# Kernel tuning notes

Hardware: AMD Instinct MI355X
Metric: run time of the kernel (lower is better)

Reference implementation:

```python
import jax, jax.numpy as jnp
import numpy as np

D = 256; NH = 8; NL = 4; NP = 4; DH = D // NH; DFFN = 1024; NQ = 900; BS = 4
SPATIAL = ((92, 92), (46, 46), (23, 23), (12, 12))  # (H, W) per level
LEVEL_START = (0, 8464, 10580, 11109)
S = sum(h * w for h, w in SPATIAL)  # 11253


def _ln(x, g, b):
    m = jnp.mean(x, -1, keepdims=True)
    v = jnp.var(x, -1, keepdims=True)
    return (x - m) / jnp.sqrt(v + 1e-5) * g + b


def setup_inputs() -> dict:
    key = jax.random.key(0)
    ks = jax.random.split(key, 24)
    p = lambda k, s: 0.02 * jax.random.normal(k, s, jnp.float32)
    return {
        "tgt": jax.random.normal(ks[0], (NQ, BS, D), jnp.float32),
        "tgt_query_pos": jax.random.normal(ks[1], (NQ, BS, D), jnp.float32),
        "tgt_reference_points": jax.random.uniform(ks[2], (NQ, BS, NL, 2), jnp.float32),
        "memory": jax.random.normal(ks[3], (S, BS, D), jnp.float32),
        "memory_spatial_shapes": jnp.array(SPATIAL, jnp.int32),
        "memory_level_start_index": jnp.array(LEVEL_START, jnp.int32),
        "in_proj_w": p(ks[4], (3 * D, D)), "in_proj_b": p(ks[5], (3 * D,)),
        "out_proj_w": p(ks[6], (D, D)), "out_proj_b": p(ks[7], (D,)),
        "off_w": p(ks[8], (NH * NL * NP * 2, D)), "off_b": p(ks[9], (NH * NL * NP * 2,)),
        "aw_w": p(ks[10], (NH * NL * NP, D)), "aw_b": p(ks[11], (NH * NL * NP,)),
        "vproj_w": p(ks[12], (D, D)), "vproj_b": p(ks[13], (D,)),
        "oproj_w": p(ks[14], (D, D)), "oproj_b": p(ks[15], (D,)),
        "ln1_g": jnp.ones((D,), jnp.float32), "ln1_b": jnp.zeros((D,), jnp.float32),
        "ln2_g": jnp.ones((D,), jnp.float32), "ln2_b": jnp.zeros((D,), jnp.float32),
        "ln3_g": jnp.ones((D,), jnp.float32), "ln3_b": jnp.zeros((D,), jnp.float32),
        "lin1_w": p(ks[16], (DFFN, D)), "lin1_b": p(ks[17], (DFFN,)),
        "lin2_w": p(ks[18], (D, DFFN)), "lin2_b": p(ks[19], (D,)),
    }


def _self_attn(q, k, v, in_w, in_b, out_w, out_b):
    # q, k, v: (nq, bs, d) -- torch nn.MultiheadAttention, eval mode
    wq, wk, wv = jnp.split(in_w, 3, axis=0)
    bq, bk, bv = jnp.split(in_b, 3)
    qp = (q @ wq.T + bq).reshape(NQ, BS, NH, DH)
    kp = (k @ wk.T + bk).reshape(NQ, BS, NH, DH)
    vp = (v @ wv.T + bv).reshape(NQ, BS, NH, DH)
    s = jnp.einsum("qbhd,kbhd->bhqk", qp, kp) / jnp.sqrt(jnp.float32(DH))
    a = jax.nn.softmax(s, axis=-1)
    o = jnp.einsum("bhqk,kbhd->qbhd", a, vp).reshape(NQ, BS, D)
    return o @ out_w.T + out_b


def _msdeform(x, ref, mem, off_w, off_b, aw_w, aw_b, vproj_w, vproj_b, oproj_w, oproj_b):
    # x: (bs, nq, d); ref: (bs, nq, nl, 2) in [0,1]; mem: (bs, S, d)
    value = (mem @ vproj_w.T + vproj_b).reshape(BS, S, NH, DH)
    off = (x @ off_w.T + off_b).reshape(BS, NQ, NH, NL, NP, 2)
    aw = jax.nn.softmax((x @ aw_w.T + aw_b).reshape(BS, NQ, NH, NL * NP), axis=-1)
    aw = aw.reshape(BS, NQ, NH, NL, NP)
    # offset normalizer = (W, H) per level
    norm = jnp.array([[w, h] for (h, w) in SPATIAL], jnp.float32)
    loc = ref[:, :, None, :, None, :] + off / norm[None, None, None, :, None, :]
    out = jnp.zeros((BS, NH, NQ, DH), x.dtype)
    for l, (H, W) in enumerate(SPATIAL):
        s0 = LEVEL_START[l]
        v = value[:, s0:s0 + H * W].transpose(0, 2, 1, 3)  # (bs, nh, H*W, dh)
        g = loc[:, :, :, l].transpose(0, 2, 1, 3, 4)       # (bs, nh, nq, np, 2)
        # grid_sample align_corners=False, padding_mode='zeros'
        px = g[..., 0] * W - 0.5
        py = g[..., 1] * H - 0.5
        x0 = jnp.floor(px).astype(jnp.int32)
        y0 = jnp.floor(py).astype(jnp.int32)
        wx = px - x0
        wy = py - y0
        samp = jnp.zeros((BS, NH, NQ, NP, DH), x.dtype)
        for dx, dy, w in ((0, 0, (1 - wx) * (1 - wy)), (1, 0, wx * (1 - wy)),
                          (0, 1, (1 - wx) * wy), (1, 1, wx * wy)):
            xi = x0 + dx
            yi = y0 + dy
            valid = ((xi >= 0) & (xi < W) & (yi >= 0) & (yi < H)).astype(x.dtype)
            idx = (jnp.clip(yi, 0, H - 1) * W + jnp.clip(xi, 0, W - 1)).reshape(BS, NH, NQ * NP)
            gat = jnp.take_along_axis(v, idx[..., None], axis=2).reshape(BS, NH, NQ, NP, DH)
            samp = samp + (w * valid)[..., None] * gat
        a = aw[:, :, :, l].transpose(0, 2, 1, 3)  # (bs, nh, nq, np)
        out = out + (samp * a[..., None]).sum(axis=3)
    out = out.transpose(0, 2, 1, 3).reshape(BS, NQ, D)
    return out @ oproj_w.T + oproj_b


def reference(tgt, tgt_query_pos, tgt_reference_points, memory,
              memory_spatial_shapes, memory_level_start_index,
              in_proj_w, in_proj_b, out_proj_w, out_proj_b,
              off_w, off_b, aw_w, aw_b, vproj_w, vproj_b, oproj_w, oproj_b,
              ln1_g, ln1_b, ln2_g, ln2_b, ln3_g, ln3_b,
              lin1_w, lin1_b, lin2_w, lin2_b):
    # module_seq = ['sa', 'ca', 'ffn']; dropout inactive (eval)
    q = tgt + tgt_query_pos
    tgt2 = _self_attn(q, q, tgt, in_proj_w, in_proj_b, out_proj_w, out_proj_b)
    tgt = _ln(tgt + tgt2, ln2_g, ln2_b)
    x = (tgt + tgt_query_pos).transpose(1, 0, 2)
    ref = tgt_reference_points.transpose(1, 0, 2, 3)
    mem = memory.transpose(1, 0, 2)
    tgt2 = _msdeform(x, ref, mem, off_w, off_b, aw_w, aw_b,
                     vproj_w, vproj_b, oproj_w, oproj_b).transpose(1, 0, 2)
    tgt = _ln(tgt + tgt2, ln1_g, ln1_b)
    ff = jax.nn.relu(tgt @ lin1_w.T + lin1_b) @ lin2_w.T + lin2_b
    return _ln(tgt + ff, ln3_g, ln3_b)
```

## Files before the change

kernel.cpp:

```cpp
#include <hip/hip_runtime.h>
#include <math.h>

#define D_MODEL 256
#define NHEAD   8
#define NLVL    4
#define NPTS    4
#define DHEAD   32
#define DFFN    1024
#define NQ      900
#define BSZ     4
#define NROW    (NQ * BSZ)
#define S_TOT   11253
#define VROWS   (S_TOT * BSZ)
#define SASCALE 0.17677669529663687f

typedef __attribute__((ext_vector_type(8))) short short8;
typedef __attribute__((ext_vector_type(4))) float f32x4;
typedef unsigned short ushort_t;

static __device__ __forceinline__ unsigned f2bf1(float f) {
    unsigned u = __float_as_uint(f);
    return (u + 0x7FFFu + ((u >> 16) & 1u)) >> 16;
}
static __device__ __forceinline__ unsigned pack2bf(float x, float y) {
    return f2bf1(x) | (f2bf1(y) << 16);
}
static __device__ __forceinline__ float bf2f(ushort_t u) {
    return __uint_as_float(((unsigned)u) << 16);
}

#define GPAD 72

__global__ __launch_bounds__(256) void qkv_fused(
    const float* __restrict__ tgt, const float* __restrict__ qpos,
    const float* __restrict__ W, const float* __restrict__ bias,
    ushort_t* __restrict__ C)
{
    __shared__ ushort_t As[64 * GPAD];
    __shared__ ushort_t Ws[64 * GPAD];

    const int t  = threadIdx.x;
    const int m0 = blockIdx.x * 64;
    const int n0 = blockIdx.y * 64;
    const bool addpos = (n0 < 512);
    const float oscale = (n0 < 256) ? SASCALE : 1.f;

    const int trow = t >> 2;
    const int tk   = (t & 3) << 4;
    const int wv   = t >> 6;
    const int ln   = t & 63;
    const int L    = ln & 15;
    const int quad = ln >> 4;

    f32x4 acc[4] = {{0.f,0.f,0.f,0.f},{0.f,0.f,0.f,0.f},
                    {0.f,0.f,0.f,0.f},{0.f,0.f,0.f,0.f}};

    for (int k0 = 0; k0 < 256; k0 += 64) {
        {
            int m = m0 + trow;
            float4 a0, a1, a2, a3;
            if (m < NROW) {
                const float* ap = tgt + (size_t)m * 256 + k0 + tk;
                a0 = *(const float4*)(ap + 0);
                a1 = *(const float4*)(ap + 4);
                a2 = *(const float4*)(ap + 8);
                a3 = *(const float4*)(ap + 12);
                if (addpos) {
                    const float* pp = qpos + (size_t)m * 256 + k0 + tk;
                    float4 p0 = *(const float4*)(pp + 0);
                    float4 p1 = *(const float4*)(pp + 4);
                    float4 p2 = *(const float4*)(pp + 8);
                    float4 p3 = *(const float4*)(pp + 12);
                    a0.x += p0.x; a0.y += p0.y; a0.z += p0.z; a0.w += p0.w;
                    a1.x += p1.x; a1.y += p1.y; a1.z += p1.z; a1.w += p1.w;
                    a2.x += p2.x; a2.y += p2.y; a2.z += p2.z; a2.w += p2.w;
                    a3.x += p3.x; a3.y += p3.y; a3.z += p3.z; a3.w += p3.w;
                }
            } else {
                a0 = a1 = a2 = a3 = make_float4(0.f, 0.f, 0.f, 0.f);
            }
            uint4 u0, u1;
            u0.x = pack2bf(a0.x, a0.y); u0.y = pack2bf(a0.z, a0.w);
            u0.z = pack2bf(a1.x, a1.y); u0.w = pack2bf(a1.z, a1.w);
            u1.x = pack2bf(a2.x, a2.y); u1.y = pack2bf(a2.z, a2.w);
            u1.z = pack2bf(a3.x, a3.y); u1.w = pack2bf(a3.z, a3.w);
            *(uint4*)&As[trow * GPAD + tk + 0] = u0;
            *(uint4*)&As[trow * GPAD + tk + 8] = u1;
        }
        {
            int n = n0 + trow;
            const float* wp = W + (size_t)n * 256 + k0 + tk;
            float4 a0 = *(const float4*)(wp + 0);
            float4 a1 = *(const float4*)(wp + 4);
            float4 a2 = *(const float4*)(wp + 8);
            float4 a3 = *(const float4*)(wp + 12);
            uint4 u0, u1;
            u0.x = pack2bf(a0.x, a0.y); u0.y = pack2bf(a0.z, a0.w);
            u0.z = pack2bf(a1.x, a1.y); u0.w = pack2bf(a1.z, a1.w);
            u1.x = pack2bf(a2.x, a2.y); u1.y = pack2bf(a2.z, a2.w);
            u1.z = pack2bf(a3.x, a3.y); u1.w = pack2bf(a3.z, a3.w);
            *(uint4*)&Ws[trow * GPAD + tk + 0] = u0;
            *(uint4*)&Ws[trow * GPAD + tk + 8] = u1;
        }
        __syncthreads();
#pragma unroll
        for (int kh = 0; kh < 2; ++kh) {
            short8 af = *(const short8*)&As[(wv * 16 + L) * GPAD + kh * 32 + quad * 8];
#pragma unroll
            for (int cb = 0; cb < 4; ++cb) {
                short8 bf = *(const short8*)&Ws[(cb * 16 + L) * GPAD + kh * 32 + quad * 8];
                acc[cb] = __builtin_amdgcn_mfma_f32_16x16x32_bf16(af, bf, acc[cb], 0, 0, 0);
            }
        }
        __syncthreads();
    }
#pragma unroll
    for (int cb = 0; cb < 4; ++cb) {
        int col = n0 + cb * 16 + L;
        float bv = bias[col];
#pragma unroll
        for (int i = 0; i < 4; ++i) {
            int m = m0 + wv * 16 + quad * 4 + i;
            if (m < NROW)
                C[(size_t)m * 768 + col] = (ushort_t)f2bf1((acc[cb][i] + bv) * oscale);
        }
    }
}

__global__ __launch_bounds__(256) void sa_flash16(
    const ushort_t* __restrict__ qkv, ushort_t* __restrict__ attn_out)
{
    __shared__ ushort_t Ks[2 * 2080];
    __shared__ ushort_t Vt[2 * 2304];
    __shared__ ushort_t Ps[4 * 1152];

    const int t    = threadIdx.x;
    const int q0   = blockIdx.x * 64;
    const int b    = blockIdx.y & 3;
    const int h    = blockIdx.y >> 2;
    const int wv   = t >> 6;
    const int ln   = t & 63;
    const int L    = ln & 15;
    const int quad = ln >> 4;

    union { uint4 u; short8 s; } qu;
    qu.u = make_uint4(0u, 0u, 0u, 0u);
    {
        int q = q0 + wv * 16 + L;
        if (q < NQ)
            qu.u = *(const uint4*)(qkv + ((size_t)q * 4 + b) * 768 + h * 32 + quad * 8);
    }
    const short8 qf = qu.s;

    float mrun = -1e30f, lrun = 0.f;
    f32x4 oacc[2] = {{0.f,0.f,0.f,0.f},{0.f,0.f,0.f,0.f}};

    const int skey = t >> 2;
    const int sdg  = t & 3;

    int it = 0;
    for (int k0 = 0; k0 < NQ; k0 += 64, it ^= 1) {
        {
            int kg = k0 + skey;
            uint4 ku = make_uint4(0u,0u,0u,0u), vu = make_uint4(0u,0u,0u,0u);
            if (kg < NQ) {
                const ushort_t* base = qkv + ((size_t)kg * 4 + b) * 768 + 256 + h * 32 + sdg * 8;
                ku = *(const uint4*)base;
                vu = *(const uint4*)(base + 256);
            }
            *(uint4*)&Ks[it * 2080 + sdg * 520 + skey * 8] = ku;
            ushort_t* vp = &Vt[it * 2304 + sdg * 8 * 72 + skey];
            vp[0 * 72] = (ushort_t)(vu.x & 0xffffu);
            vp[1 * 72] = (ushort_t)(vu.x >> 16);
            vp[2 * 72] = (ushort_t)(vu.y & 0xffffu);
            vp[3 * 72] = (ushort_t)(vu.y >> 16);
            vp[4 * 72] = (ushort_t)(vu.z & 0xffffu);
            vp[5 * 72] = (ushort_t)(vu.z >> 16);
            vp[6 * 72] = (ushort_t)(vu.w & 0xffffu);
            vp[7 * 72] = (ushort_t)(vu.w >> 16);
        }
        __syncthreads();

        f32x4 sacc[4] = {{0.f,0.f,0.f,0.f},{0.f,0.f,0.f,0.f},
                         {0.f,0.f,0.f,0.f},{0.f,0.f,0.f,0.f}};
#pragma unroll
        for (int cb = 0; cb < 4; ++cb) {
            short8 kf = *(const short8*)&Ks[it * 2080 + quad * 520 + (cb * 16 + L) * 8];
            sacc[cb] = __builtin_amdgcn_mfma_f32_16x16x32_bf16(kf, qf, sacc[cb], 0, 0, 0);
        }
        if (k0 + 64 > NQ) {
#pragma unroll
            for (int cb = 0; cb < 4; ++cb)
#pragma unroll
                for (int i = 0; i < 4; ++i)
                    if (k0 + cb * 16 + quad * 4 + i >= NQ) sacc[cb][i] = -1e30f;
        }

        float ml = -1e30f;
#pragma unroll
        for (int cb = 0; cb < 4; ++cb)
#pragma unroll
            for (int i = 0; i < 4; ++i) ml = fmaxf(ml, sacc[cb][i]);
        ml = fmaxf(ml, __shfl_xor(ml, 16, 64));
        ml = fmaxf(ml, __shfl_xor(ml, 32, 64));
        float mnew  = fmaxf(mrun, ml);
        float alpha = __expf(mrun - mnew);
        float p[16];
        float rs = 0.f;
#pragma unroll
        for (int cb = 0; cb < 4; ++cb)
#pragma unroll
            for (int i = 0; i < 4; ++i) {
                float e = __expf(sacc[cb][i] - mnew);
                p[cb * 4 + i] = e;
                rs += e;
            }
        rs += __shfl_xor(rs, 16, 64);
        rs += __shfl_xor(rs, 32, 64);
        lrun = lrun * alpha + rs;
        mrun = mnew;

        {
            ushort_t* pw = &Ps[wv * 1152 + L * 72];
#pragma unroll
            for (int cb = 0; cb < 4; ++cb) {
                uint2 u;
                u.x = pack2bf(p[cb * 4 + 0], p[cb * 4 + 1]);
                u.y = pack2bf(p[cb * 4 + 2], p[cb * 4 + 3]);
                *(uint2*)&pw[cb * 16 + quad * 4] = u;
            }
        }
#pragma unroll
        for (int i = 0; i < 4; ++i) {
            float ai = __shfl(alpha, quad * 4 + i, 64);
            oacc[0][i] *= ai;
            oacc[1][i] *= ai;
        }
        __syncthreads();

#pragma unroll
        for (int ks = 0; ks < 2; ++ks) {
            short8 pf = *(const short8*)&Ps[wv * 1152 + L * 72 + ks * 32 + quad * 8];
#pragma unroll
            for (int db = 0; db < 2; ++db) {
                short8 vf = *(const short8*)&Vt[it * 2304 + (db * 16 + L) * 72 + ks * 32 + quad * 8];
                oacc[db] = __builtin_amdgcn_mfma_f32_16x16x32_bf16(pf, vf, oacc[db], 0, 0, 0);
            }
        }
    }

#pragma unroll
    for (int i = 0; i < 4; ++i) {
        float lq = __shfl(lrun, quad * 4 + i, 64);
        float li = 1.f / lq;
        int q = q0 + wv * 16 + quad * 4 + i;
        if (q < NQ) {
            ushort_t* op = attn_out + ((size_t)q * 4 + b) * 256 + h * 32 + L;
            op[0]  = (ushort_t)f2bf1(oacc[0][i] * li);
            op[16] = (ushort_t)f2bf1(oacc[1][i] * li);
        }
    }
}

__global__ __launch_bounds__(256) void gemm16_f32(
    const ushort_t* __restrict__ A, const float* __restrict__ W,
    const float* __restrict__ bias, float* __restrict__ C,
    int M, int N, int K, int ldc)
{
    __shared__ ushort_t As[64 * GPAD];
    __shared__ ushort_t Ws[64 * GPAD];

    const int t  = threadIdx.x;
    const int m0 = blockIdx.x * 64;
    const int n0 = blockIdx.y * 64;
    const int trow = t >> 2;
    const int tk   = (t & 3) << 4;
    const int wv   = t >> 6;
    const int ln   = t & 63;
    const int L    = ln & 15;
    const int quad = ln >> 4;

    f32x4 acc[4] = {{0.f,0.f,0.f,0.f},{0.f,0.f,0.f,0.f},
                    {0.f,0.f,0.f,0.f},{0.f,0.f,0.f,0.f}};

    for (int k0 = 0; k0 < K; k0 += 64) {
        {
            int m = m0 + trow;
            uint4 a0 = make_uint4(0u,0u,0u,0u), a1 = make_uint4(0u,0u,0u,0u);
            if (m < M) {
                const ushort_t* ap = A + (size_t)m * K + k0 + tk;
                a0 = *(const uint4*)ap;
                a1 = *(const uint4*)(ap + 8);
            }
            *(uint4*)&As[trow * GPAD + tk + 0] = a0;
            *(uint4*)&As[trow * GPAD + tk + 8] = a1;
        }
        {
            int n = n0 + trow;
            const float* wp = W + (size_t)n * K + k0 + tk;
            float4 a0 = *(const float4*)(wp + 0);
            float4 a1 = *(const float4*)(wp + 4);
            float4 a2 = *(const float4*)(wp + 8);
            float4 a3 = *(const float4*)(wp + 12);
            uint4 u0, u1;
            u0.x = pack2bf(a0.x, a0.y); u0.y = pack2bf(a0.z, a0.w);
            u0.z = pack2bf(a1.x, a1.y); u0.w = pack2bf(a1.z, a1.w);
            u1.x = pack2bf(a2.x, a2.y); u1.y = pack2bf(a2.z, a2.w);
            u1.z = pack2bf(a3.x, a3.y); u1.w = pack2bf(a3.z, a3.w);
            *(uint4*)&Ws[trow * GPAD + tk + 0] = u0;
            *(uint4*)&Ws[trow * GPAD + tk + 8] = u1;
        }
        __syncthreads();
#pragma unroll
        for (int kh = 0; kh < 2; ++kh) {
            short8 af = *(const short8*)&As[(wv * 16 + L) * GPAD + kh * 32 + quad * 8];
#pragma unroll
            for (int cb = 0; cb < 4; ++cb) {
                short8 bf = *(const short8*)&Ws[(cb * 16 + L) * GPAD + kh * 32 + quad * 8];
                acc[cb] = __builtin_amdgcn_mfma_f32_16x16x32_bf16(af, bf, acc[cb], 0, 0, 0);
            }
        }
        __syncthreads();
    }
#pragma unroll
    for (int cb = 0; cb < 4; ++cb) {
        int col = n0 + cb * 16 + L;
        float bv = bias[col];
#pragma unroll
        for (int i = 0; i < 4; ++i) {
            int m = m0 + wv * 16 + quad * 4 + i;
            if (m < M)
                C[(size_t)m * ldc + col] = acc[cb][i] + bv;
        }
    }
}

__global__ __launch_bounds__(256) void ln_resid16(
    const float* __restrict__ xa, const float* __restrict__ xb,
    const float* __restrict__ gam, const float* __restrict__ bet,
    float* __restrict__ out, const float* __restrict__ pos,
    ushort_t* __restrict__ out2)
{
    const int row = blockIdx.x;
    const int t = threadIdx.x;
    float x = xa[(size_t)row * D_MODEL + t] + xb[(size_t)row * D_MODEL + t];
    float s = x, s2 = x * x;
#pragma unroll
    for (int off = 32; off > 0; off >>= 1) {
        s  += __shfl_down(s, off, 64);
        s2 += __shfl_down(s2, off, 64);
    }
    __shared__ float rs[4], rs2[4];
    __shared__ float mean_s, rstd_s;
    int wid = t >> 6, lane = t & 63;
    if (lane == 0) { rs[wid] = s; rs2[wid] = s2; }
    __syncthreads();
    if (t == 0) {
        float S = rs[0] + rs[1] + rs[2] + rs[3];
        float S2 = rs2[0] + rs2[1] + rs2[2] + rs2[3];
        float mean = S * (1.f / 256.f);
        float var = S2 * (1.f / 256.f) - mean * mean;
        mean_s = mean;
        rstd_s = rsqrtf(var + 1e-5f);
    }
    __syncthreads();
    float y = (x - mean_s) * rstd_s * gam[t] + bet[t];
    out[(size_t)row * D_MODEL + t] = y;
    if (out2) {
        float o2 = y + (pos ? pos[(size_t)row * D_MODEL + t] : 0.f);
        out2[(size_t)row * D_MODEL + t] = (ushort_t)f2bf1(o2);
    }
}

__global__ __launch_bounds__(256) void vproj_bf16(
    const float* __restrict__ A, const float* __restrict__ W,
    const float* __restrict__ bias, ushort_t* __restrict__ C, int M)
{
    __shared__ ushort_t As[64 * GPAD];
    __shared__ ushort_t Ws[256 * GPAD];

    const int t  = threadIdx.x;
    const int m0 = blockIdx.x * 64;
    const int trow = t >> 2;
    const int tk   = (t & 3) << 4;
    const int wv   = t >> 6;
    const int ln   = t & 63;
    const int L    = ln & 15;
    const int quad = ln >> 4;

    f32x4 acc[16];
#pragma unroll
    for (int i = 0; i < 16; ++i) acc[i] = (f32x4){0.f, 0.f, 0.f, 0.f};

    for (int k0 = 0; k0 < 256; k0 += 64) {
        {
            int m = m0 + trow;
            float4 a0, a1, a2, a3;
            if (m < M) {
                const float* ap = A + (size_t)m * 256 + k0 + tk;
                a0 = *(const float4*)(ap + 0);
                a1 = *(const float4*)(ap + 4);
                a2 = *(const float4*)(ap + 8);
                a3 = *(const float4*)(ap + 12);
            } else {
                a0 = a1 = a2 = a3 = make_float4(0.f, 0.f, 0.f, 0.f);
            }
            uint4 u0, u1;
            u0.x = pack2bf(a0.x, a0.y); u0.y = pack2bf(a0.z, a0.w);
            u0.z = pack2bf(a1.x, a1.y); u0.w = pack2bf(a1.z, a1.w);
            u1.x = pack2bf(a2.x, a2.y); u1.y = pack2bf(a2.z, a2.w);
            u1.z = pack2bf(a3.x, a3.y); u1.w = pack2bf(a3.z, a3.w);
            *(uint4*)&As[trow * GPAD + tk + 0] = u0;
            *(uint4*)&As[trow * GPAD + tk + 8] = u1;
        }
#pragma unroll
        for (int wb = 0; wb < 4; ++wb) {
            int n = wb * 64 + trow;
            const float* wp = W + (size_t)n * 256 + k0 + tk;
            float4 a0 = *(const float4*)(wp + 0);
            float4 a1 = *(const float4*)(wp + 4);
            float4 a2 = *(const float4*)(wp + 8);
            float4 a3 = *(const float4*)(wp + 12);
            uint4 u0, u1;
            u0.x = pack2bf(a0.x, a0.y); u0.y = pack2bf(a0.z, a0.w);
            u0.z = pack2bf(a1.x, a1.y); u0.w = pack2bf(a1.z, a1.w);
            u1.x = pack2bf(a2.x, a2.y); u1.y = pack2bf(a2.z, a2.w);
            u1.z = pack2bf(a3.x, a3.y); u1.w = pack2bf(a3.z, a3.w);
            *(uint4*)&Ws[n * GPAD + tk + 0] = u0;
            *(uint4*)&Ws[n * GPAD + tk + 8] = u1;
        }
        __syncthreads();
#pragma unroll
        for (int kh = 0; kh < 2; ++kh) {
            short8 af = *(const short8*)&As[(wv * 16 + L) * GPAD + kh * 32 + quad * 8];
#pragma unroll
            for (int cb = 0; cb < 16; ++cb) {
                short8 bf = *(const short8*)&Ws[(cb * 16 + L) * GPAD + kh * 32 + quad * 8];
                acc[cb] = __builtin_amdgcn_mfma_f32_16x16x32_bf16(af, bf, acc[cb], 0, 0, 0);
            }
        }
        __syncthreads();
    }

    ushort_t* Cs = Ws;
#pragma unroll
    for (int cb = 0; cb < 16; ++cb) {
        int col = cb * 16 + L;
        float bv = bias[col];
#pragma unroll
        for (int i = 0; i < 4; ++i) {
            int r = wv * 16 + quad * 4 + i;
            Cs[r * 264 + col] = (ushort_t)f2bf1(acc[cb][i] + bv);
        }
    }
    __syncthreads();
    {
        int r  = t >> 2;
        int ch = (t & 3) * 64;
        int m  = m0 + r;
        if (m < M) {
            const ushort_t* src = &Cs[r * 264 + ch];
            uint4* dst = (uint4*)(C + (size_t)m * 256 + ch);
#pragma unroll
            for (int j = 0; j < 8; ++j)
                dst[j] = *(const uint4*)(src + j * 8);
        }
    }
}

__global__ __launch_bounds__(256) void offaw16(
    const ushort_t* __restrict__ A,
    const float* __restrict__ off_w, const float* __restrict__ off_b,
    const float* __restrict__ aw_w, const float* __restrict__ aw_b,
    float* __restrict__ off_raw, float* __restrict__ aw_raw)
{
    __shared__ ushort_t As[64 * GPAD];
    __shared__ ushort_t Ws[64 * GPAD];

    const int t  = threadIdx.x;
    const int m0 = blockIdx.x * 64;
    const int by = blockIdx.y;
    const bool isaw = (by >= 4);
    const int n0 = isaw ? (by - 4) * 64 : by * 64;
    const float* W  = isaw ? aw_w : off_w;
    const float* bs = isaw ? aw_b : off_b;
    float* C = isaw ? aw_raw : off_raw;
    const int ldc = isaw ? 128 : 256;

    const int trow = t >> 2;
    const int tk   = (t & 3) << 4;
    const int wv   = t >> 6;
    const int ln   = t & 63;
    const int L    = ln & 15;
    const int quad = ln >> 4;

    f32x4 acc[4] = {{0.f,0.f,0.f,0.f},{0.f,0.f,0.f,0.f},
                    {0.f,0.f,0.f,0.f},{0.f,0.f,0.f,0.f}};

    for (int k0 = 0; k0 < 256; k0 += 64) {
        {
            int m = m0 + trow;
            uint4 a0 = make_uint4(0u,0u,0u,0u), a1 = make_uint4(0u,0u,0u,0u);
            if (m < NROW) {
                const ushort_t* ap = A + (size_t)m * 256 + k0 + tk;
                a0 = *(const uint4*)ap;
                a1 = *(const uint4*)(ap + 8);
            }
            *(uint4*)&As[trow * GPAD + tk + 0] = a0;
            *(uint4*)&As[trow * GPAD + tk + 8] = a1;
        }
        {
            int n = n0 + trow;
            const float* wp = W + (size_t)n * 256 + k0 + tk;
            float4 a0 = *(const float4*)(wp + 0);
            float4 a1 = *(const float4*)(wp + 4);
            float4 a2 = *(const float4*)(wp + 8);
            float4 a3 = *(const float4*)(wp + 12);
            uint4 u0, u1;
            u0.x = pack2bf(a0.x, a0.y); u0.y = pack2bf(a0.z, a0.w);
            u0.z = pack2bf(a1.x, a1.y); u0.w = pack2bf(a1.z, a1.w);
            u1.x = pack2bf(a2.x, a2.y); u1.y = pack2bf(a2.z, a2.w);
            u1.z = pack2bf(a3.x, a3.y); u1.w = pack2bf(a3.z, a3.w);
            *(uint4*)&Ws[trow * GPAD + tk + 0] = u0;
            *(uint4*)&Ws[trow * GPAD + tk + 8] = u1;
        }
        __syncthreads();
#pragma unroll
        for (int kh = 0; kh < 2; ++kh) {
            short8 af = *(const short8*)&As[(wv * 16 + L) * GPAD + kh * 32 + quad * 8];
#pragma unroll
            for (int cb = 0; cb < 4; ++cb) {
                short8 bf = *(const short8*)&Ws[(cb * 16 + L) * GPAD + kh * 32 + quad * 8];
                acc[cb] = __builtin_amdgcn_mfma_f32_16x16x32_bf16(af, bf, acc[cb], 0, 0, 0);
            }
        }
        __syncthreads();
    }
#pragma unroll
    for (int cb = 0; cb < 4; ++cb) {
        int col = n0 + cb * 16 + L;
        float bv = bs[col];
#pragma unroll
        for (int i = 0; i < 4; ++i) {
            int m = m0 + wv * 16 + quad * 4 + i;
            if (m < NROW)
                C[(size_t)m * ldc + col] = acc[cb][i] + bv;
        }
    }
}

__global__ __launch_bounds__(256) void gemm16_16(
    const ushort_t* __restrict__ A, const float* __restrict__ W,
    const float* __restrict__ bias, ushort_t* __restrict__ C,
    int M, int N, int K, int ldc, int relu)
{
    __shared__ ushort_t As[64 * GPAD];
    __shared__ ushort_t Ws[64 * GPAD];

    const int t  = threadIdx.x;
    const int m0 = blockIdx.x * 64;
    const int n0 = blockIdx.y * 64;
    const int trow = t >> 2;
    const int tk   = (t & 3) << 4;
    const int wv   = t >> 6;
    const int ln   = t & 63;
    const int L    = ln & 15;
    const int quad = ln >> 4;

    f32x4 acc[4] = {{0.f,0.f,0.f,0.f},{0.f,0.f,0.f,0.f},
                    {0.f,0.f,0.f,0.f},{0.f,0.f,0.f,0.f}};

    for (int k0 = 0; k0 < K; k0 += 64) {
        {
            int m = m0 + trow;
            uint4 a0 = make_uint4(0u,0u,0u,0u), a1 = make_uint4(0u,0u,0u,0u);
            if (m < M) {
                const ushort_t* ap = A + (size_t)m * K + k0 + tk;
                a0 = *(const uint4*)ap;
                a1 = *(const uint4*)(ap + 8);
            }
            *(uint4*)&As[trow * GPAD + tk + 0] = a0;
            *(uint4*)&As[trow * GPAD + tk + 8] = a1;
        }
        {
            int n = n0 + trow;
            const float* wp = W + (size_t)n * K + k0 + tk;
            float4 a0 = *(const float4*)(wp + 0);
            float4 a1 = *(const float4*)(wp + 4);
            float4 a2 = *(const float4*)(wp + 8);
            float4 a3 = *(const float4*)(wp + 12);
            uint4 u0, u1;
            u0.x = pack2bf(a0.x, a0.y); u0.y = pack2bf(a0.z, a0.w);
            u0.z = pack2bf(a1.x, a1.y); u0.w = pack2bf(a1.z, a1.w);
            u1.x = pack2bf(a2.x, a2.y); u1.y = pack2bf(a2.z, a2.w);
            u1.z = pack2bf(a3.x, a3.y); u1.w = pack2bf(a3.z, a3.w);
            *(uint4*)&Ws[trow * GPAD + tk + 0] = u0;
            *(uint4*)&Ws[trow * GPAD + tk + 8] = u1;
        }
        __syncthreads();
#pragma unroll
        for (int kh = 0; kh < 2; ++kh) {
            short8 af = *(const short8*)&As[(wv * 16 + L) * GPAD + kh * 32 + quad * 8];
#pragma unroll
            for (int cb = 0; cb < 4; ++cb) {
                short8 bf = *(const short8*)&Ws[(cb * 16 + L) * GPAD + kh * 32 + quad * 8];
                acc[cb] = __builtin_amdgcn_mfma_f32_16x16x32_bf16(af, bf, acc[cb], 0, 0, 0);
            }
        }
        __syncthreads();
    }
#pragma unroll
    for (int cb = 0; cb < 4; ++cb) {
        int col = n0 + cb * 16 + L;
        float bv = bias[col];
#pragma unroll
        for (int i = 0; i < 4; ++i) {
            int m = m0 + wv * 16 + quad * 4 + i;
            if (m < M) {
                float o = acc[cb][i] + bv;
                if (relu) o = fmaxf(o, 0.f);
                C[(size_t)m * ldc + col] = (ushort_t)f2bf1(o);
            }
        }
    }
}

__global__ __launch_bounds__(256) void msdeform16(
    const float* __restrict__ off_raw, const float* __restrict__ aw_raw,
    const float* __restrict__ refp, const ushort_t* __restrict__ value,
    ushort_t* __restrict__ out)
{
    const int row = blockIdx.x;
    const int b = row & 3;
    const int t = threadIdx.x;

    __shared__ float aw_s[8][17];
    __shared__ float px_s[8][16];
    __shared__ float py_s[8][16];

    const int Hs[4]  = {92, 46, 23, 12};
    const int Wd[4]  = {92, 46, 23, 12};
    const int S0_[4] = {0, 8464, 10580, 11109};

    if (t < 128) {
        int hh = t >> 4, lp = t & 15, l = lp >> 2;
        float ox = off_raw[(size_t)row * 256 + hh * 32 + lp * 2 + 0];
        float oy = off_raw[(size_t)row * 256 + hh * 32 + lp * 2 + 1];
        float rx = refp[((size_t)row * 4 + l) * 2 + 0];
        float ry = refp[((size_t)row * 4 + l) * 2 + 1];
        px_s[hh][lp] = rx * (float)Wd[l] + ox - 0.5f;
        py_s[hh][lp] = ry * (float)Hs[l] + oy - 0.5f;
    }
    if (t < 8) {
        int hh = t;
        float v[16];
        float m = -1e30f;
#pragma unroll
        for (int j = 0; j < 16; ++j) {
            v[j] = aw_raw[(size_t)row * 128 + hh * 16 + j];
            m = fmaxf(m, v[j]);
        }
        float ssum = 0.f;
#pragma unroll
        for (int j = 0; j < 16; ++j) { v[j] = __expf(v[j] - m); ssum += v[j]; }
        float inv = 1.f / ssum;
#pragma unroll
        for (int j = 0; j < 16; ++j) aw_s[hh][j] = v[j] * inv;
    }
    __syncthreads();

    const int h = t >> 5, d = t & 31;
    const ushort_t* vb = value + (size_t)b * 256 + h * 32 + d;
    float acc = 0.f;
#pragma unroll
    for (int l = 0; l < 4; ++l) {
        const int H = Hs[l], W = Wd[l], base = S0_[l];
#pragma unroll
        for (int p = 0; p < 4; ++p) {
            const int lp = l * 4 + p;
            float px = px_s[h][lp], py = py_s[h][lp];
            float x0f = floorf(px), y0f = floorf(py);
            int x0 = (int)x0f, y0 = (int)y0f;
            float wx = px - x0f, wy = py - y0f;
            float sv = 0.f;
#pragma unroll
            for (int dy = 0; dy < 2; ++dy) {
#pragma unroll
                for (int dx = 0; dx < 2; ++dx) {
                    int xi = x0 + dx, yi = y0 + dy;
                    float flag = (xi >= 0 && xi < W && yi >= 0 && yi < H) ? 1.f : 0.f;
                    int xc = xi < 0 ? 0 : (xi >= W ? W - 1 : xi);
                    int yc = yi < 0 ? 0 : (yi >= H ? H - 1 : yi);
                    float wgt = (dx ? wx : 1.f - wx) * (dy ? wy : 1.f - wy);
                    float gv = bf2f(vb[(size_t)(base + yc * W + xc) * 1024]);
                    sv = fmaf(wgt * flag, gv, sv);
                }
            }
            acc = fmaf(aw_s[h][lp], sv, acc);
        }
    }
    out[(size_t)row * 256 + h * 32 + d] = (ushort_t)f2bf1(acc);
}

extern "C" void kernel_launch(void* const* d_in, const int* in_sizes, int n_in,
                              void* d_out, int out_size, void* d_ws, size_t ws_size,
                              hipStream_t stream)
{
    const float* tgt    = (const float*)d_in[0];
    const float* qpos   = (const float*)d_in[1];
    const float* refp   = (const float*)d_in[2];
    const float* mem    = (const float*)d_in[3];
    const float* in_w   = (const float*)d_in[6];
    const float* in_b   = (const float*)d_in[7];
    const float* outp_w = (const float*)d_in[8];
    const float* outp_b = (const float*)d_in[9];
    const float* off_w  = (const float*)d_in[10];
    const float* off_b  = (const float*)d_in[11];
    const float* aw_w   = (const float*)d_in[12];
    const float* aw_b   = (const float*)d_in[13];
    const float* vp_w   = (const float*)d_in[14];
    const float* vp_b   = (const float*)d_in[15];
    const float* op_w   = (const float*)d_in[16];
    const float* op_b   = (const float*)d_in[17];
    const float* ln1g   = (const float*)d_in[18];
    const float* ln1b   = (const float*)d_in[19];
    const float* ln2g   = (const float*)d_in[20];
    const float* ln2b   = (const float*)d_in[21];
    const float* ln3g   = (const float*)d_in[22];
    const float* ln3b   = (const float*)d_in[23];
    const float* l1w    = (const float*)d_in[24];
    const float* l1b    = (const float*)d_in[25];
    const float* l2w    = (const float*)d_in[26];
    const float* l2b    = (const float*)d_in[27];
    float* out = (float*)d_out;
    float* ws  = (float*)d_ws;

    ushort_t* qkv16   = (ushort_t*)ws;
    ushort_t* att16   = (ushort_t*)(ws + 1382400);
    float*    tgt_a   = ws + 1843200;
    ushort_t* xca16   = (ushort_t*)(ws + 2764800);
    float*    off_raw = ws + 3225600;
    float*    aw_raw  = ws + 4147200;
    ushort_t* att2_16 = (ushort_t*)(ws + 4608000);
    float*    tgt_b   = ws + 5068800;
    ushort_t* tgtb16  = (ushort_t*)(ws + 5990400);
    ushort_t* value16 = (ushort_t*)(ws + 6451200);
    ushort_t* hidden16= (ushort_t*)(ws + 12212736);
    float*    tmp     = ws + 14055936;

    dim3 b256(256);

    hipLaunchKernelGGL(qkv_fused, dim3(57, 12), b256, 0, stream,
                       tgt, qpos, in_w, in_b, qkv16);
    hipLaunchKernelGGL(sa_flash16, dim3(15, 32), b256, 0, stream, qkv16, att16);
    hipLaunchKernelGGL(gemm16_f32, dim3(57, 4), b256, 0, stream,
                       att16, outp_w, outp_b, tmp, NROW, 256, 256, 256);
    hipLaunchKernelGGL(ln_resid16, dim3(3600), b256, 0, stream,
                       tgt, tmp, ln2g, ln2b, tgt_a, qpos, xca16);
    hipLaunchKernelGGL(vproj_bf16, dim3(704), b256, 0, stream,
                       mem, vp_w, vp_b, value16, VROWS);
    hipLaunchKernelGGL(offaw16, dim3(57, 6), b256, 0, stream,
                       xca16, off_w, off_b, aw_w, aw_b, off_raw, aw_raw);
    hipLaunchKernelGGL(msdeform16, dim3(3600), b256, 0, stream,
                       off_raw, aw_raw, refp, value16, att2_16);
    hipLaunchKernelGGL(gemm16_f32, dim3(57, 4), b256, 0, stream,
                       att2_16, op_w, op_b, tmp, NROW, 256, 256, 256);
    hipLaunchKernelGGL(ln_resid16, dim3(3600), b256, 0, stream,
                       tgt_a, tmp, ln1g, ln1b, tgt_b, (const float*)nullptr, tgtb16);
    hipLaunchKernelGGL(gemm16_16, dim3(57, 16), b256, 0, stream,
                       tgtb16, l1w, l1b, hidden16, NROW, 1024, 256, 1024, 1);
    hipLaunchKernelGGL(gemm16_f32, dim3(57, 4), b256, 0, stream,
                       hidden16, l2w, l2b, tmp, NROW, 256, 1024, 256);
    hipLaunchKernelGGL(ln_resid16, dim3(3600), b256, 0, stream,
                       tgt_b, tmp, ln3g, ln3b, out, (const float*)nullptr, (ushort_t*)nullptr);
}
```

Before: 290.9 us.

## Merge QKV projection and value projection into one launch

Combines the self-attention QKV GEMM and the memory value-projection GEMM into a single kernel that dispatches on block index, so the two independent GEMMs share one grid. This removes one kernel launch and lets the value projection run alongside the QKV blocks instead of after the self-attention stages. The shared-memory allocation grows to the larger 256-row weight tile for all blocks, which may reduce occupancy for the QKV blocks. Workspace offsets are also repacked.

```diff
diff --git a/kernel.cpp b/kernel.cpp
--- a/kernel.cpp
+++ b/kernel.cpp
@@ -31,20 +31,18 @@
 
 #define GPAD 72
 
-__global__ __launch_bounds__(256) void qkv_fused(
+__global__ __launch_bounds__(256) void proj_fused(
     const float* __restrict__ tgt, const float* __restrict__ qpos,
-    const float* __restrict__ W, const float* __restrict__ bias,
-    ushort_t* __restrict__ C)
+    const float* __restrict__ in_w, const float* __restrict__ in_b,
+    const float* __restrict__ mem, const float* __restrict__ vp_w,
+    const float* __restrict__ vp_b,
+    ushort_t* __restrict__ qkv16, ushort_t* __restrict__ value16)
 {
     __shared__ ushort_t As[64 * GPAD];
-    __shared__ ushort_t Ws[64 * GPAD];
-
-    const int t  = threadIdx.x;
-    const int m0 = blockIdx.x * 64;
-    const int n0 = blockIdx.y * 64;
-    const bool addpos = (n0 < 512);
-    const float oscale = (n0 < 256) ? SASCALE : 1.f;
-
+    __shared__ ushort_t Ws[256 * GPAD];
+
+    const int t    = threadIdx.x;
+    const int bid  = blockIdx.x;
     const int trow = t >> 2;
     const int tk   = (t & 3) << 4;
     const int wv   = t >> 6;
@@ -52,77 +50,165 @@
     const int L    = ln & 15;
     const int quad = ln >> 4;
 
-    f32x4 acc[4] = {{0.f,0.f,0.f,0.f},{0.f,0.f,0.f,0.f},
-                    {0.f,0.f,0.f,0.f},{0.f,0.f,0.f,0.f}};
-
-    for (int k0 = 0; k0 < 256; k0 += 64) {
-        {
-            int m = m0 + trow;
-            float4 a0, a1, a2, a3;
-            if (m < NROW) {
-                const float* ap = tgt + (size_t)m * 256 + k0 + tk;
-                a0 = *(const float4*)(ap + 0);
-                a1 = *(const float4*)(ap + 4);
-                a2 = *(const float4*)(ap + 8);
-                a3 = *(const float4*)(ap + 12);
-                if (addpos) {
-                    const float* pp = qpos + (size_t)m * 256 + k0 + tk;
-                    float4 p0 = *(const float4*)(pp + 0);
-                    float4 p1 = *(const float4*)(pp + 4);
-                    float4 p2 = *(const float4*)(pp + 8);
-                    float4 p3 = *(const float4*)(pp + 12);
-                    a0.x += p0.x; a0.y += p0.y; a0.z += p0.z; a0.w += p0.w;
-                    a1.x += p1.x; a1.y += p1.y; a1.z += p1.z; a1.w += p1.w;
-                    a2.x += p2.x; a2.y += p2.y; a2.z += p2.z; a2.w += p2.w;
-                    a3.x += p3.x; a3.y += p3.y; a3.z += p3.z; a3.w += p3.w;
+    if (bid < 684) {
+        const int m0 = (bid % 57) * 64;
+        const int n0 = (bid / 57) * 64;
+        const bool addpos = (n0 < 512);
+        const float oscale = (n0 < 256) ? SASCALE : 1.f;
+
+        f32x4 acc[4] = {{0.f,0.f,0.f,0.f},{0.f,0.f,0.f,0.f},
+                        {0.f,0.f,0.f,0.f},{0.f,0.f,0.f,0.f}};
+
+        for (int k0 = 0; k0 < 256; k0 += 64) {
+            {
+                int m = m0 + trow;
+                float4 a0, a1, a2, a3;
+                if (m < NROW) {
+                    const float* ap = tgt + (size_t)m * 256 + k0 + tk;
+                    a0 = *(const float4*)(ap + 0);
+                    a1 = *(const float4*)(ap + 4);
+                    a2 = *(const float4*)(ap + 8);
+                    a3 = *(const float4*)(ap + 12);
+                    if (addpos) {
+                        const float* pp = qpos + (size_t)m * 256 + k0 + tk;
+                        float4 p0 = *(const float4*)(pp + 0);
+                        float4 p1 = *(const float4*)(pp + 4);
+                        float4 p2 = *(const float4*)(pp + 8);
+                        float4 p3 = *(const float4*)(pp + 12);
+                        a0.x += p0.x; a0.y += p0.y; a0.z += p0.z; a0.w += p0.w;
+                        a1.x += p1.x; a1.y += p1.y; a1.z += p1.z; a1.w += p1.w;
+                        a2.x += p2.x; a2.y += p2.y; a2.z += p2.z; a2.w += p2.w;
+                        a3.x += p3.x; a3.y += p3.y; a3.z += p3.z; a3.w += p3.w;
+                    }
+                } else {
+                    a0 = a1 = a2 = a3 = make_float4(0.f, 0.f, 0.f, 0.f);
                 }
-            } else {
-                a0 = a1 = a2 = a3 = make_float4(0.f, 0.f, 0.f, 0.f);
-            }
-            uint4 u0, u1;
-            u0.x = pack2bf(a0.x, a0.y); u0.y = pack2bf(a0.z, a0.w);
-            u0.z = pack2bf(a1.x, a1.y); u0.w = pack2bf(a1.z, a1.w);
-            u1.x = pack2bf(a2.x, a2.y); u1.y = pack2bf(a2.z, a2.w);
-            u1.z = pack2bf(a3.x, a3.y); u1.w = pack2bf(a3.z, a3.w);
-            *(uint4*)&As[trow * GPAD + tk + 0] = u0;
-            *(uint4*)&As[trow * GPAD + tk + 8] = u1;
-        }
-        {
-            int n = n0 + trow;
-            const float* wp = W + (size_t)n * 256 + k0 + tk;
-            float4 a0 = *(const float4*)(wp + 0);
-            float4 a1 = *(const float4*)(wp + 4);
-            float4 a2 = *(const float4*)(wp + 8);
-            float4 a3 = *(const float4*)(wp + 12);
-            uint4 u0, u1;
-            u0.x = pack2bf(a0.x, a0.y); u0.y = pack2bf(a0.z, a0.w);
-            u0.z = pack2bf(a1.x, a1.y); u0.w = pack2bf(a1.z, a1.w);
-            u1.x = pack2bf(a2.x, a2.y); u1.y = pack2bf(a2.z, a2.w);
-            u1.z = pack2bf(a3.x, a3.y); u1.w = pack2bf(a3.z, a3.w);
-            *(uint4*)&Ws[trow * GPAD + tk + 0] = u0;
-            *(uint4*)&Ws[trow * GPAD + tk + 8] = u1;
-        }
-        __syncthreads();
-#pragma unroll
-        for (int kh = 0; kh < 2; ++kh) {
-            short8 af = *(const short8*)&As[(wv * 16 + L) * GPAD + kh * 32 + quad * 8];
-#pragma unroll
-            for (int cb = 0; cb < 4; ++cb) {
-                short8 bf = *(const short8*)&Ws[(cb * 16 + L) * GPAD + kh * 32 + quad * 8];
-                acc[cb] = __builtin_amdgcn_mfma_f32_16x16x32_bf16(af, bf, acc[cb], 0, 0, 0);
-            }
-        }
-        __syncthreads();
-    }
-#pragma unroll
-    for (int cb = 0; cb < 4; ++cb) {
-        int col = n0 + cb * 16 + L;
-        float bv = bias[col];
-#pragma unroll
-        for (int i = 0; i < 4; ++i) {
-            int m = m0 + wv * 16 + quad * 4 + i;
-            if (m < NROW)
-                C[(size_t)m * 768 + col] = (ushort_t)f2bf1((acc[cb][i] + bv) * oscale);
+                uint4 u0, u1;
+                u0.x = pack2bf(a0.x, a0.y); u0.y = pack2bf(a0.z, a0.w);
+                u0.z = pack2bf(a1.x, a1.y); u0.w = pack2bf(a1.z, a1.w);
+                u1.x = pack2bf(a2.x, a2.y); u1.y = pack2bf(a2.z, a2.w);
+                u1.z = pack2bf(a3.x, a3.y); u1.w = pack2bf(a3.z, a3.w);
+                *(uint4*)&As[trow * GPAD + tk + 0] = u0;
+                *(uint4*)&As[trow * GPAD + tk + 8] = u1;
+            }
+            {
+                int n = n0 + trow;
+                const float* wp = in_w + (size_t)n * 256 + k0 + tk;
+                float4 a0 = *(const float4*)(wp + 0);
+                float4 a1 = *(const float4*)(wp + 4);
+                float4 a2 = *(const float4*)(wp + 8);
+                float4 a3 = *(const float4*)(wp + 12);
+                uint4 u0, u1;
+                u0.x = pack2bf(a0.x, a0.y); u0.y = pack2bf(a0.z, a0.w);
+                u0.z = pack2bf(a1.x, a1.y); u0.w = pack2bf(a1.z, a1.w);
+                u1.x = pack2bf(a2.x, a2.y); u1.y = pack2bf(a2.z, a2.w);
+                u1.z = pack2bf(a3.x, a3.y); u1.w = pack2bf(a3.z, a3.w);
+                *(uint4*)&Ws[trow * GPAD + tk + 0] = u0;
+                *(uint4*)&Ws[trow * GPAD + tk + 8] = u1;
+            }
+            __syncthreads();
+#pragma unroll
+            for (int kh = 0; kh < 2; ++kh) {
+                short8 af = *(const short8*)&As[(wv * 16 + L) * GPAD + kh * 32 + quad * 8];
+#pragma unroll
+                for (int cb = 0; cb < 4; ++cb) {
+                    short8 bf = *(const short8*)&Ws[(cb * 16 + L) * GPAD + kh * 32 + quad * 8];
+                    acc[cb] = __builtin_amdgcn_mfma_f32_16x16x32_bf16(af, bf, acc[cb], 0, 0, 0);
+                }
+            }
+            __syncthreads();
+        }
+#pragma unroll
+        for (int cb = 0; cb < 4; ++cb) {
+            int col = n0 + cb * 16 + L;
+            float bv = in_b[col];
+#pragma unroll
+            for (int i = 0; i < 4; ++i) {
+                int m = m0 + wv * 16 + quad * 4 + i;
+                if (m < NROW)
+                    qkv16[(size_t)m * 768 + col] = (ushort_t)f2bf1((acc[cb][i] + bv) * oscale);
+            }
+        }
+    } else {
+        const int m0 = (bid - 684) * 64;
+
+        f32x4 acc[16];
+#pragma unroll
+        for (int i = 0; i < 16; ++i) acc[i] = (f32x4){0.f, 0.f, 0.f, 0.f};
+
+        for (int k0 = 0; k0 < 256; k0 += 64) {
+            {
+                int m = m0 + trow;
+                float4 a0, a1, a2, a3;
+                if (m < VROWS) {
+                    const float* ap = mem + (size_t)m * 256 + k0 + tk;
+                    a0 = *(const float4*)(ap + 0);
+                    a1 = *(const float4*)(ap + 4);
+                    a2 = *(const float4*)(ap + 8);
+                    a3 = *(const float4*)(ap + 12);
+                } else {
+                    a0 = a1 = a2 = a3 = make_float4(0.f, 0.f, 0.f, 0.f);
+                }
+                uint4 u0, u1;
+                u0.x = pack2bf(a0.x, a0.y); u0.y = pack2bf(a0.z, a0.w);
+                u0.z = pack2bf(a1.x, a1.y); u0.w = pack2bf(a1.z, a1.w);
+                u1.x = pack2bf(a2.x, a2.y); u1.y = pack2bf(a2.z, a2.w);
+                u1.z = pack2bf(a3.x, a3.y); u1.w = pack2bf(a3.z, a3.w);
+                *(uint4*)&As[trow * GPAD + tk + 0] = u0;
+                *(uint4*)&As[trow * GPAD + tk + 8] = u1;
+            }
+#pragma unroll
+            for (int wb = 0; wb < 4; ++wb) {
+                int n = wb * 64 + trow;
+                const float* wp = vp_w + (size_t)n * 256 + k0 + tk;
+                float4 a0 = *(const float4*)(wp + 0);
+                float4 a1 = *(const float4*)(wp + 4);
+                float4 a2 = *(const float4*)(wp + 8);
+                float4 a3 = *(const float4*)(wp + 12);
+                uint4 u0, u1;
+                u0.x = pack2bf(a0.x, a0.y); u0.y = pack2bf(a0.z, a0.w);
+                u0.z = pack2bf(a1.x, a1.y); u0.w = pack2bf(a1.z, a1.w);
+                u1.x = pack2bf(a2.x, a2.y); u1.y = pack2bf(a2.z, a2.w);
+                u1.z = pack2bf(a3.x, a3.y); u1.w = pack2bf(a3.z, a3.w);
+                *(uint4*)&Ws[n * GPAD + tk + 0] = u0;
+                *(uint4*)&Ws[n * GPAD + tk + 8] = u1;
+            }
+            __syncthreads();
+#pragma unroll
+            for (int kh = 0; kh < 2; ++kh) {
+                short8 af = *(const short8*)&As[(wv * 16 + L) * GPAD + kh * 32 + quad * 8];
+#pragma unroll
+                for (int cb = 0; cb < 16; ++cb) {
+                    short8 bf = *(const short8*)&Ws[(cb * 16 + L) * GPAD + kh * 32 + quad * 8];
+                    acc[cb] = __builtin_amdgcn_mfma_f32_16x16x32_bf16(af, bf, acc[cb], 0, 0, 0);
+                }
+            }
+            __syncthreads();
+        }
+
+        ushort_t* Cs = Ws;
+#pragma unroll
+        for (int cb = 0; cb < 16; ++cb) {
+            int col = cb * 16 + L;
+            float bv = vp_b[col];
+#pragma unroll
+            for (int i = 0; i < 4; ++i) {
+                int r = wv * 16 + quad * 4 + i;
+                Cs[r * 264 + col] = (ushort_t)f2bf1(acc[cb][i] + bv);
+            }
+        }
+        __syncthreads();
+        {
+            int r  = t >> 2;
+            int ch = (t & 3) * 64;
+            int m  = m0 + r;
+            if (m < VROWS) {
+                const ushort_t* src = &Cs[r * 264 + ch];
+                uint4* dst = (uint4*)(value16 + (size_t)m * 256 + ch);
+#pragma unroll
+                for (int j = 0; j < 8; ++j)
+                    dst[j] = *(const uint4*)(src + j * 8);
+            }
         }
     }
 }
@@ -369,102 +455,6 @@
     if (out2) {
         float o2 = y + (pos ? pos[(size_t)row * D_MODEL + t] : 0.f);
         out2[(size_t)row * D_MODEL + t] = (ushort_t)f2bf1(o2);
-    }
-}
-
-__global__ __launch_bounds__(256) void vproj_bf16(
-    const float* __restrict__ A, const float* __restrict__ W,
-    const float* __restrict__ bias, ushort_t* __restrict__ C, int M)
-{
-    __shared__ ushort_t As[64 * GPAD];
-    __shared__ ushort_t Ws[256 * GPAD];
-
-    const int t  = threadIdx.x;
-    const int m0 = blockIdx.x * 64;
-    const int trow = t >> 2;
-    const int tk   = (t & 3) << 4;
-    const int wv   = t >> 6;
-    const int ln   = t & 63;
-    const int L    = ln & 15;
-    const int quad = ln >> 4;
-
-    f32x4 acc[16];
-#pragma unroll
-    for (int i = 0; i < 16; ++i) acc[i] = (f32x4){0.f, 0.f, 0.f, 0.f};
-
-    for (int k0 = 0; k0 < 256; k0 += 64) {
-        {
-            int m = m0 + trow;
-            float4 a0, a1, a2, a3;
-            if (m < M) {
-                const float* ap = A + (size_t)m * 256 + k0 + tk;
-                a0 = *(const float4*)(ap + 0);
-                a1 = *(const float4*)(ap + 4);
-                a2 = *(const float4*)(ap + 8);
-                a3 = *(const float4*)(ap + 12);
-            } else {
-                a0 = a1 = a2 = a3 = make_float4(0.f, 0.f, 0.f, 0.f);
-            }
-            uint4 u0, u1;
-            u0.x = pack2bf(a0.x, a0.y); u0.y = pack2bf(a0.z, a0.w);
-            u0.z = pack2bf(a1.x, a1.y); u0.w = pack2bf(a1.z, a1.w);
-            u1.x = pack2bf(a2.x, a2.y); u1.y = pack2bf(a2.z, a2.w);
-            u1.z = pack2bf(a3.x, a3.y); u1.w = pack2bf(a3.z, a3.w);
-            *(uint4*)&As[trow * GPAD + tk + 0] = u0;
-            *(uint4*)&As[trow * GPAD + tk + 8] = u1;
-        }
-#pragma unroll
-        for (int wb = 0; wb < 4; ++wb) {
-            int n = wb * 64 + trow;
-            const float* wp = W + (size_t)n * 256 + k0 + tk;
-            float4 a0 = *(const float4*)(wp + 0);
-            float4 a1 = *(const float4*)(wp + 4);
-            float4 a2 = *(const float4*)(wp + 8);
-            float4 a3 = *(const float4*)(wp + 12);
-            uint4 u0, u1;
-            u0.x = pack2bf(a0.x, a0.y); u0.y = pack2bf(a0.z, a0.w);
-            u0.z = pack2bf(a1.x, a1.y); u0.w = pack2bf(a1.z, a1.w);
-            u1.x = pack2bf(a2.x, a2.y); u1.y = pack2bf(a2.z, a2.w);
-            u1.z = pack2bf(a3.x, a3.y); u1.w = pack2bf(a3.z, a3.w);
-            *(uint4*)&Ws[n * GPAD + tk + 0] = u0;
-            *(uint4*)&Ws[n * GPAD + tk + 8] = u1;
-        }
-        __syncthreads();
-#pragma unroll
-        for (int kh = 0; kh < 2; ++kh) {
-            short8 af = *(const short8*)&As[(wv * 16 + L) * GPAD + kh * 32 + quad * 8];
-#pragma unroll
-            for (int cb = 0; cb < 16; ++cb) {
-                short8 bf = *(const short8*)&Ws[(cb * 16 + L) * GPAD + kh * 32 + quad * 8];
-                acc[cb] = __builtin_amdgcn_mfma_f32_16x16x32_bf16(af, bf, acc[cb], 0, 0, 0);
-            }
-        }
-        __syncthreads();
-    }
-
-    ushort_t* Cs = Ws;
-#pragma unroll
-    for (int cb = 0; cb < 16; ++cb) {
-        int col = cb * 16 + L;
-        float bv = bias[col];
-#pragma unroll
-        for (int i = 0; i < 4; ++i) {
-            int r = wv * 16 + quad * 4 + i;
-            Cs[r * 264 + col] = (ushort_t)f2bf1(acc[cb][i] + bv);
-        }
-    }
-    __syncthreads();
-    {
-        int r  = t >> 2;
-        int ch = (t & 3) * 64;
-        int m  = m0 + r;
-        if (m < M) {
-            const ushort_t* src = &Cs[r * 264 + ch];
-            uint4* dst = (uint4*)(C + (size_t)m * 256 + ch);
-#pragma unroll
-            for (int j = 0; j < 8; ++j)
-                dst[j] = *(const uint4*)(src + j * 8);
-        }
     }
 }
 
@@ -735,30 +725,28 @@
     float* out = (float*)d_out;
     float* ws  = (float*)d_ws;
 
-    ushort_t* qkv16   = (ushort_t*)ws;
-    ushort_t* att16   = (ushort_t*)(ws + 1382400);
-    float*    tgt_a   = ws + 1843200;
-    ushort_t* xca16   = (ushort_t*)(ws + 2764800);
-    float*    off_raw = ws + 3225600;
-    float*    aw_raw  = ws + 4147200;
-    ushort_t* att2_16 = (ushort_t*)(ws + 4608000);
-    float*    tgt_b   = ws + 5068800;
-    ushort_t* tgtb16  = (ushort_t*)(ws + 5990400);
-    ushort_t* value16 = (ushort_t*)(ws + 6451200);
-    ushort_t* hidden16= (ushort_t*)(ws + 12212736);
-    float*    tmp     = ws + 14055936;
+    ushort_t* qkv16    = (ushort_t*)ws;
+    ushort_t* att16    = (ushort_t*)(ws + 691200);
+    float*    tmp      = ws + 921600;
+    float*    tgt_a    = ws + 1843200;
+    ushort_t* xca16    = (ushort_t*)(ws + 2764800);
+    float*    off_raw  = ws + 2995200;
+    float*    aw_raw   = ws + 3916800;
+    ushort_t* att2_16  = (ushort_t*)(ws + 4377600);
+    float*    tgt_b    = ws + 4608000;
+    ushort_t* tgtb16   = (ushort_t*)(ws + 5529600);
+    ushort_t* value16  = (ushort_t*)(ws + 5760000);
+    ushort_t* hidden16 = (ushort_t*)(ws + 11521536);
 
     dim3 b256(256);
 
-    hipLaunchKernelGGL(qkv_fused, dim3(57, 12), b256, 0, stream,
-                       tgt, qpos, in_w, in_b, qkv16);
+    hipLaunchKernelGGL(proj_fused, dim3(1388), b256, 0, stream,
+                       tgt, qpos, in_w, in_b, mem, vp_w, vp_b, qkv16, value16);
     hipLaunchKernelGGL(sa_flash16, dim3(15, 32), b256, 0, stream, qkv16, att16);
     hipLaunchKernelGGL(gemm16_f32, dim3(57, 4), b256, 0, stream,
                        att16, outp_w, outp_b, tmp, NROW, 256, 256, 256);
     hipLaunchKernelGGL(ln_resid16, dim3(3600), b256, 0, stream,
                        tgt, tmp, ln2g, ln2b, tgt_a, qpos, xca16);
-    hipLaunchKernelGGL(vproj_bf16, dim3(704), b256, 0, stream,
-                       mem, vp_w, vp_b, value16, VROWS);
     hipLaunchKernelGGL(offaw16, dim3(57, 6), b256, 0, stream,
                        xca16, off_w, off_b, aw_w, aw_b, off_raw, aw_raw);
     hipLaunchKernelGGL(msdeform16, dim3(3600), b256, 0, stream,
```

New measurement: 292.3 us. Within noise of the previous version (+0.5%).
